# Kernel optimization log

Hardware: AMD Instinct MI355X
Metric: run time of the kernel (lower is better)

The kernel has to match this reference:

```python
import jax, jax.numpy as jnp
import numpy as np

CELL = 128
STEPS = 20
N_KEYS = 4   # ['first_conn','second_conn','first_op','second_op']
N_OUT = 6


def setup_inputs() -> dict:
    key = jax.random.key(0)
    ks = jax.random.split(key, 10)
    s = 0.05
    return {
        "net": jax.random.randint(ks[0], (STEPS,), 0, N_OUT),          # sampled actions, each in [0,6)
        "reward": jax.random.uniform(ks[1], (1,), dtype=jnp.float32),   # unused in forward (kept for signature parity)
        "emb_start": jax.random.normal(ks[2], (1, CELL), jnp.float32) * s,          # Embedding(1,128)
        "emb_keys": jax.random.normal(ks[3], (N_KEYS, N_OUT, CELL), jnp.float32) * s,
        "fc_W": jax.random.normal(ks[4], (N_KEYS, N_OUT, CELL), jnp.float32) * s,
        "fc_b": jax.random.normal(ks[5], (N_KEYS, N_OUT), jnp.float32) * s,
        "W_ih": jax.random.normal(ks[6], (4 * CELL, CELL), jnp.float32) * s,  # LSTMCell input weights (i,f,g,o)
        "W_hh": jax.random.normal(ks[7], (4 * CELL, CELL), jnp.float32) * s,  # LSTMCell hidden weights
        "b_ih": jax.random.normal(ks[8], (4 * CELL,), jnp.float32) * s,
        "b_hh": jax.random.normal(ks[9], (4 * CELL,), jnp.float32) * s,
    }


def _lstm_cell(x, h, c, W_ih, W_hh, b_ih, b_hh):
    # PyTorch LSTMCell: gates ordered (i, f, g, o)
    gates = x @ W_ih.T + b_ih + h @ W_hh.T + b_hh   # [1, 4*CELL]
    i, f, g, o = jnp.split(gates, 4, axis=-1)
    c_new = jax.nn.sigmoid(f) * c + jax.nn.sigmoid(i) * jnp.tanh(g)
    h_new = jax.nn.sigmoid(o) * jnp.tanh(c_new)
    return h_new, c_new


def reference(net, reward, emb_start, emb_keys, fc_W, fc_b, W_ih, W_hh, b_ih, b_hh):
    key_idx = jnp.arange(STEPS) % N_KEYS            # which head/embedding at each step
    fc_W_t = fc_W[key_idx]                          # [STEPS, 6, CELL]
    fc_b_t = fc_b[key_idx]                          # [STEPS, 6]
    emb_t = emb_keys[key_idx, net]                  # [STEPS, CELL] next-step input embedding

    def step(carry, xs):
        h, c, x = carry
        Wt, bt, ev = xs
        h, c = _lstm_cell(x, h, c, W_ih, W_hh, b_ih, b_hh)
        probs = jax.nn.softmax(h @ Wt.T + bt, axis=1)   # [1, 6]
        return (h, c, ev[None, :]), probs

    h0 = jnp.zeros((1, CELL), dtype=emb_start.dtype)
    c0 = jnp.zeros((1, CELL), dtype=emb_start.dtype)
    x0 = emb_start                                   # embedding lookup of action 0 in a 1-row table
    _, outputs = jax.lax.scan(step, (h0, c0, x0), (fc_W_t, fc_b_t, emb_t))
    return outputs                                   # [STEPS, 1, 6], stacked version of the torch list
```

## Files before the change

### kernel.cpp

```cpp
#include <hip/hip_runtime.h>
#include <hip/hip_fp16.h>

#define CELL 128
#define STEPS 20

typedef _Float16 half8_t __attribute__((ext_vector_type(8)));
typedef float    floatx4 __attribute__((ext_vector_type(4)));

#define WS_GX    0
#define WS_WHH   40960
#define WS_FCW   (40960 + 131072)
#define WS_FCB   (WS_FCW + 6144)
#define WS_NEED  (WS_FCB + 96)

__device__ __forceinline__ unsigned packf2(float x, float y) {
    typedef _Float16 h2 __attribute__((ext_vector_type(2)));
    h2 h = { (_Float16)x, (_Float16)y };
    return __builtin_bit_cast(unsigned, h);
}
__device__ __forceinline__ float fdot2u(unsigned a, unsigned b, float c) {
    typedef _Float16 h2 __attribute__((ext_vector_type(2)));
#if __has_builtin(__builtin_amdgcn_fdot2)
    return __builtin_amdgcn_fdot2(__builtin_bit_cast(h2, a), __builtin_bit_cast(h2, b), c, false);
#else
    h2 x = __builtin_bit_cast(h2, a), y = __builtin_bit_cast(h2, b);
    return fmaf((float)x[0], (float)y[0], fmaf((float)x[1], (float)y[1], c));
#endif
}
__device__ __forceinline__ float fastrcp(float x) {
#if __has_builtin(__builtin_amdgcn_rcpf)
    return __builtin_amdgcn_rcpf(x);
#else
    return 1.0f / x;
#endif
}
__device__ __forceinline__ float sig_rcp(float x)  { return fastrcp(1.0f + __expf(-x)); }
__device__ __forceinline__ float tanh_rcp(float x) { return fmaf(2.0f, fastrcp(1.0f + __expf(-2.0f * x)), -1.0f); }
__device__ __forceinline__ half8_t cvt8(const float* p) {
    const float4* p4 = (const float4*)p;
    float4 a = p4[0], b = p4[1];
    return half8_t{ (_Float16)a.x, (_Float16)a.y, (_Float16)a.z, (_Float16)a.w,
                    (_Float16)b.x, (_Float16)b.y, (_Float16)b.z, (_Float16)b.w };
}

extern "C" __global__ void __launch_bounds__(256)
nas_prep_kernel(const int* __restrict__ net,
                const float* __restrict__ emb_start,
                const float* __restrict__ emb_keys,
                const float* __restrict__ fc_W,
                const float* __restrict__ fc_b,
                const float* __restrict__ W_ih,
                const float* __restrict__ W_hh,
                const float* __restrict__ b_ih,
                const float* __restrict__ b_hh,
                unsigned char* __restrict__ ws)
{
    const int b = blockIdx.x, tid = threadIdx.x;

    if (b < 128) {
        __shared__ float sx[STEPS][CELL];
        for (int i = tid; i < STEPS * CELL; i += 256) {
            const int t = i >> 7, k = i & 127;
            sx[t][k] = (t == 0) ? emb_start[k]
                     : emb_keys[((((t - 1) & 3) * 6) + net[t - 1]) * CELL + k];
        }
        __syncthreads();
        const int row  = b * 4 + (tid >> 6);
        const int lane = tid & 63;
        const float2 w = ((const float2*)W_ih)[row * 64 + lane];
        const float bias = b_ih[row] + b_hh[row];
        const int tau = row >> 7, cell = row & 127;
        float* gx = (float*)(ws + WS_GX);
#pragma unroll
        for (int t = 0; t < STEPS; ++t) {
            const float2 xv = *(const float2*)&sx[t][lane * 2];
            float p = fmaf(w.x, xv.x, w.y * xv.y);
            p += __shfl_down(p, 32); p += __shfl_down(p, 16);
            p += __shfl_down(p, 8);  p += __shfl_down(p, 4);
            p += __shfl_down(p, 2);  p += __shfl_down(p, 1);
            if (lane == 0) gx[t * 512 + cell * 4 + tau] = p + bias;
        }
    } else if (b < 160) {
        const int F   = (b - 128) * 256 + tid;
        const int g   = F >> 9;
        const int m   = F & 511;
        const int tau = g >> 2, kc = g & 3;
        const int rr0 = ((m >> 6) << 4) + (m & 15);
        const int qd  = (m >> 4) & 3;
        const int k0  = kc * 32 + qd * 8;
        half8_t h8 = cvt8(W_hh + (tau * 128 + rr0) * CELL + k0);
        ((uint4*)(ws + WS_WHH))[g * 512 + m] = __builtin_bit_cast(uint4, h8);
    } else {
        const float2* fw2 = (const float2*)fc_W;
        unsigned* fcw = (unsigned*)(ws + WS_FCW);
        for (int i = tid; i < 24 * 64; i += 256) {
            const float2 w = fw2[i];
            fcw[i] = packf2(w.x, w.y);
        }
        if (tid < 24) ((float*)(ws + WS_FCB))[tid] = fc_b[tid];
    }
}

extern "C" __global__ void __launch_bounds__(512, 1)
nas_policy_kernel(const unsigned char* __restrict__ ws,
                  float* __restrict__ out)
{
    const int t0   = threadIdx.x;
    const int wv   = t0 >> 6;
    const int lane = t0 & 63;
    const int quad = lane >> 4;
    const int lcol = lane & 15;
    const int rr0  = (wv << 4) + lcol;

    __shared__ __align__(16) _Float16 hbuf[2 * 128];
    __shared__ float llog[STEPS * 8];

    const float*    ws_gx  = (const float*)(ws + WS_GX);
    const uint4*    ws_whh = (const uint4*)(ws + WS_WHH);
    const unsigned* ws_fcw = (const unsigned*)(ws + WS_FCW);
    const float*    ws_fcb = (const float*)(ws + WS_FCB);

    half8_t bf0[4], bf1[4], bf2[4], bf3[4];
#pragma unroll
    for (int kc = 0; kc < 4; ++kc) {
        bf0[kc] = __builtin_bit_cast(half8_t, ws_whh[(0 * 4 + kc) * 512 + t0]);
        bf1[kc] = __builtin_bit_cast(half8_t, ws_whh[(1 * 4 + kc) * 512 + t0]);
        bf2[kc] = __builtin_bit_cast(half8_t, ws_whh[(2 * 4 + kc) * 512 + t0]);
        bf3[kc] = __builtin_bit_cast(half8_t, ws_whh[(3 * 4 + kc) * 512 + t0]);
    }
    if (t0 < 128) hbuf[128 + t0] = (_Float16)0.0f;
    floatx4 gx_cur = *(const floatx4*)&ws_gx[rr0 * 4];
    float c = 0.0f;
    __syncthreads();

    for (int t = 0; t < STEPS; ++t) {
        const uint4* hp4 = (const uint4*)(hbuf + (((t + 1) & 1) << 7));
        const floatx4 gx = gx_cur;
        if (t + 1 < STEPS)
            gx_cur = *(const floatx4*)&ws_gx[(t + 1) * 512 + rr0 * 4];

        floatx4 a0a = { gx[0], 0, 0, 0 }, a0b = { 0, 0, 0, 0 };
        floatx4 a1a = { gx[1], 0, 0, 0 }, a1b = { 0, 0, 0, 0 };
        floatx4 a2a = { gx[2], 0, 0, 0 }, a2b = { 0, 0, 0, 0 };
        floatx4 a3a = { gx[3], 0, 0, 0 }, a3b = { 0, 0, 0, 0 };
        {
            uint4 u0 = hp4[(0 << 2) + quad], u1 = hp4[(1 << 2) + quad];
            uint4 u2 = hp4[(2 << 2) + quad], u3 = hp4[(3 << 2) + quad];
            half8_t f0 = __builtin_bit_cast(half8_t, u0), f1 = __builtin_bit_cast(half8_t, u1);
            half8_t f2 = __builtin_bit_cast(half8_t, u2), f3 = __builtin_bit_cast(half8_t, u3);
            a0a = __builtin_amdgcn_mfma_f32_16x16x32_f16(f0, bf0[0], a0a, 0, 0, 0);
            a1a = __builtin_amdgcn_mfma_f32_16x16x32_f16(f0, bf1[0], a1a, 0, 0, 0);
            a2a = __builtin_amdgcn_mfma_f32_16x16x32_f16(f0, bf2[0], a2a, 0, 0, 0);
            a3a = __builtin_amdgcn_mfma_f32_16x16x32_f16(f0, bf3[0], a3a, 0, 0, 0);
            a0b = __builtin_amdgcn_mfma_f32_16x16x32_f16(f1, bf0[1], a0b, 0, 0, 0);
            a1b = __builtin_amdgcn_mfma_f32_16x16x32_f16(f1, bf1[1], a1b, 0, 0, 0);
            a2b = __builtin_amdgcn_mfma_f32_16x16x32_f16(f1, bf2[1], a2b, 0, 0, 0);
            a3b = __builtin_amdgcn_mfma_f32_16x16x32_f16(f1, bf3[1], a3b, 0, 0, 0);
            a0a = __builtin_amdgcn_mfma_f32_16x16x32_f16(f2, bf0[2], a0a, 0, 0, 0);
            a1a = __builtin_amdgcn_mfma_f32_16x16x32_f16(f2, bf1[2], a1a, 0, 0, 0);
            a2a = __builtin_amdgcn_mfma_f32_16x16x32_f16(f2, bf2[2], a2a, 0, 0, 0);
            a3a = __builtin_amdgcn_mfma_f32_16x16x32_f16(f2, bf3[2], a3a, 0, 0, 0);
            a0b = __builtin_amdgcn_mfma_f32_16x16x32_f16(f3, bf0[3], a0b, 0, 0, 0);
            a1b = __builtin_amdgcn_mfma_f32_16x16x32_f16(f3, bf1[3], a1b, 0, 0, 0);
            a2b = __builtin_amdgcn_mfma_f32_16x16x32_f16(f3, bf2[3], a2b, 0, 0, 0);
            a3b = __builtin_amdgcn_mfma_f32_16x16x32_f16(f3, bf3[3], a3b, 0, 0, 0);
        }

        if (t >= 1 && wv < 6 && quad == 1) {
            const int li = lcol;
            const int hg = ((t - 1) & 3) * 6 + wv;
            const unsigned* hb = (const unsigned*)(hbuf + (((t + 1) & 1) << 7));
            const uint4 wpv = *(const uint4*)(ws_fcw + hg * 64 + li * 4);
            float p = fdot2u(hb[li * 4],     wpv.x, 0.0f);
            p = fdot2u(hb[li * 4 + 1], wpv.y, p);
            p = fdot2u(hb[li * 4 + 2], wpv.z, p);
            p = fdot2u(hb[li * 4 + 3], wpv.w, p);
            p += __shfl_down(p, 8); p += __shfl_down(p, 4);
            p += __shfl_down(p, 2); p += __shfl_down(p, 1);
            if (li == 0) llog[(t - 1) * 8 + wv] = p + ws_fcb[hg];
        }

        {
            float ig = sig_rcp (a0a[0] + a0b[0]);
            float fg = sig_rcp (a1a[0] + a1b[0]);
            float gg = tanh_rcp(a2a[0] + a2b[0]);
            float og = sig_rcp (a3a[0] + a3b[0]);
            c = fg * c + ig * gg;
            float h = og * tanh_rcp(c);
            if (quad == 0)
                hbuf[((t & 1) << 7) + rr0] = (_Float16)h;
        }

        __syncthreads();
    }

    if (wv < 6 && quad == 1) {
        const int li = lcol;
        const int hg = (19 & 3) * 6 + wv;
        const unsigned* hb = (const unsigned*)(hbuf + 128);
        const uint4 wpv = *(const uint4*)(ws_fcw + hg * 64 + li * 4);
        float p = fdot2u(hb[li * 4],     wpv.x, 0.0f);
        p = fdot2u(hb[li * 4 + 1], wpv.y, p);
        p = fdot2u(hb[li * 4 + 2], wpv.z, p);
        p = fdot2u(hb[li * 4 + 3], wpv.w, p);
        p += __shfl_down(p, 8); p += __shfl_down(p, 4);
        p += __shfl_down(p, 2); p += __shfl_down(p, 1);
        if (li == 0) llog[19 * 8 + wv] = p + ws_fcb[hg];
    }
    __syncthreads();
    if (t0 < STEPS * 6) {
        const int s = t0 / 6, k = t0 - s * 6;
        const float* L = llog + s * 8;
        float l0 = L[0], l1 = L[1], l2 = L[2], l3 = L[3], l4 = L[4], l5 = L[5];
        float m = fmaxf(fmaxf(fmaxf(l0, l1), fmaxf(l2, l3)), fmaxf(l4, l5));
        float e0 = __expf(l0 - m), e1 = __expf(l1 - m), e2 = __expf(l2 - m);
        float e3 = __expf(l3 - m), e4 = __expf(l4 - m), e5 = __expf(l5 - m);
        float sum = ((e0 + e1) + (e2 + e3)) + (e4 + e5);
        float mine = (k == 0) ? e0 : (k == 1) ? e1 : (k == 2) ? e2
                   : (k == 3) ? e3 : (k == 4) ? e4 : e5;
        out[t0] = mine / sum;
    }
}

extern "C" __global__ void __launch_bounds__(512, 1)
nas_policy_mono(const int* __restrict__ net,
                const float* __restrict__ emb_start,
                const float* __restrict__ emb_keys,
                const float* __restrict__ fc_W,
                const float* __restrict__ fc_b,
                const float* __restrict__ W_ih,
                const float* __restrict__ W_hh,
                const float* __restrict__ b_ih,
                const float* __restrict__ b_hh,
                float* __restrict__ out)
{
    const int t0   = threadIdx.x;
    const int wv   = t0 >> 6;
    const int lane = t0 & 63;
    const int quad = lane >> 4;
    const int lcol = lane & 15;

    __shared__ __align__(16) unsigned  s_xv2[32 * 68];
    __shared__ __align__(16) float     s_gx[STEPS * 512];
    __shared__ __align__(16) _Float16  hbuf[2 * 128];
    __shared__ unsigned s_fcw2[24 * 64];
    __shared__ float    s_fcb[24];
    __shared__ float    llog[STEPS * 8];

    for (int i = t0; i < STEPS * 64; i += 512) {
        const int m = i >> 6, j = i & 63;
        const float2* src = (m == 0) ? (const float2*)emb_start
            : (const float2*)(emb_keys + ((((m - 1) & 3) * 6) + net[m - 1]) * CELL);
        float2 v = src[j];
        s_xv2[m * 68 + j] = packf2(v.x, v.y);
    }
    {
        const float2* fw2 = (const float2*)fc_W;
        for (int i = t0; i < 24 * 64; i += 512) { float2 w = fw2[i]; s_fcw2[i] = packf2(w.x, w.y); }
    }
    if (t0 < 24)  s_fcb[t0] = fc_b[t0];
    if (t0 < 128) hbuf[128 + t0] = (_Float16)0.0f;

    const int rr0 = (wv << 4) + lcol;
    float biasx[4];
#pragma unroll
    for (int tau = 0; tau < 4; ++tau) {
        const int r = tau * 128 + rr0;
        biasx[tau] = b_ih[r] + b_hh[r];
    }

    __syncthreads();

    {
        half8_t bw[4][4];
#pragma unroll
        for (int kc = 0; kc < 4; ++kc) {
            const int k0 = kc * 32 + quad * 8;
#pragma unroll
            for (int tau = 0; tau < 4; ++tau)
                bw[kc][tau] = cvt8(W_ih + (tau * 128 + rr0) * CELL + k0);
        }
        floatx4 ax0[4] = { {0,0,0,0}, {0,0,0,0}, {0,0,0,0}, {0,0,0,0} };
        floatx4 ax1[4] = { {0,0,0,0}, {0,0,0,0}, {0,0,0,0}, {0,0,0,0} };
#pragma unroll
        for (int kc = 0; kc < 4; ++kc) {
            uint4 u0 = *(const uint4*)&s_xv2[lcol * 68 + kc * 16 + quad * 4];
            uint4 u1 = *(const uint4*)&s_xv2[(16 + lcol) * 68 + kc * 16 + quad * 4];
            half8_t a0f = __builtin_bit_cast(half8_t, u0);
            half8_t a1f = __builtin_bit_cast(half8_t, u1);
#pragma unroll
            for (int tau = 0; tau < 4; ++tau) {
                ax0[tau] = __builtin_amdgcn_mfma_f32_16x16x32_f16(a0f, bw[kc][tau], ax0[tau], 0, 0, 0);
                ax1[tau] = __builtin_amdgcn_mfma_f32_16x16x32_f16(a1f, bw[kc][tau], ax1[tau], 0, 0, 0);
            }
        }
#pragma unroll
        for (int tau = 0; tau < 4; ++tau) {
#pragma unroll
            for (int reg = 0; reg < 4; ++reg)
                s_gx[(quad * 4 + reg) * 512 + rr0 * 4 + tau] = ax0[tau][reg] + biasx[tau];
            if (quad == 0) {
#pragma unroll
                for (int reg = 0; reg < 4; ++reg)
                    s_gx[(16 + reg) * 512 + rr0 * 4 + tau] = ax1[tau][reg] + biasx[tau];
            }
        }
    }

    half8_t bf0[4], bf1[4], bf2[4], bf3[4];
#pragma unroll
    for (int kc = 0; kc < 4; ++kc) {
        const int k0 = kc * 32 + quad * 8;
        bf0[kc] = cvt8(W_hh + (0 * 128 + rr0) * CELL + k0);
        bf1[kc] = cvt8(W_hh + (1 * 128 + rr0) * CELL + k0);
        bf2[kc] = cvt8(W_hh + (2 * 128 + rr0) * CELL + k0);
        bf3[kc] = cvt8(W_hh + (3 * 128 + rr0) * CELL + k0);
    }

    float c = 0.0f;
    __syncthreads();

    for (int t = 0; t < STEPS; ++t) {
        const uint4* hp4 = (const uint4*)(hbuf + (((t + 1) & 1) << 7));
        floatx4 gx = *(const floatx4*)&s_gx[t * 512 + rr0 * 4];
        floatx4 a0a = {0,0,0,0}, a0b = {0,0,0,0}, a1a = {0,0,0,0}, a1b = {0,0,0,0};
        floatx4 a2a = {0,0,0,0}, a2b = {0,0,0,0}, a3a = {0,0,0,0}, a3b = {0,0,0,0};
        {
            uint4 u0 = hp4[(0 << 2) + quad], u1 = hp4[(1 << 2) + quad];
            uint4 u2 = hp4[(2 << 2) + quad], u3 = hp4[(3 << 2) + quad];
            half8_t f0 = __builtin_bit_cast(half8_t, u0), f1 = __builtin_bit_cast(half8_t, u1);
            half8_t f2 = __builtin_bit_cast(half8_t, u2), f3 = __builtin_bit_cast(half8_t, u3);
            a0a = __builtin_amdgcn_mfma_f32_16x16x32_f16(f0, bf0[0], a0a, 0, 0, 0);
            a1a = __builtin_amdgcn_mfma_f32_16x16x32_f16(f0, bf1[0], a1a, 0, 0, 0);
            a2a = __builtin_amdgcn_mfma_f32_16x16x32_f16(f0, bf2[0], a2a, 0, 0, 0);
            a3a = __builtin_amdgcn_mfma_f32_16x16x32_f16(f0, bf3[0], a3a, 0, 0, 0);
            a0b = __builtin_amdgcn_mfma_f32_16x16x32_f16(f1, bf0[1], a0b, 0, 0, 0);
            a1b = __builtin_amdgcn_mfma_f32_16x16x32_f16(f1, bf1[1], a1b, 0, 0, 0);
            a2b = __builtin_amdgcn_mfma_f32_16x16x32_f16(f1, bf2[1], a2b, 0, 0, 0);
            a3b = __builtin_amdgcn_mfma_f32_16x16x32_f16(f1, bf3[1], a3b, 0, 0, 0);
            a0a = __builtin_amdgcn_mfma_f32_16x16x32_f16(f2, bf0[2], a0a, 0, 0, 0);
            a1a = __builtin_amdgcn_mfma_f32_16x16x32_f16(f2, bf1[2], a1a, 0, 0, 0);
            a2a = __builtin_amdgcn_mfma_f32_16x16x32_f16(f2, bf2[2], a2a, 0, 0, 0);
            a3a = __builtin_amdgcn_mfma_f32_16x16x32_f16(f2, bf3[2], a3a, 0, 0, 0);
            a0b = __builtin_amdgcn_mfma_f32_16x16x32_f16(f3, bf0[3], a0b, 0, 0, 0);
            a1b = __builtin_amdgcn_mfma_f32_16x16x32_f16(f3, bf1[3], a1b, 0, 0, 0);
            a2b = __builtin_amdgcn_mfma_f32_16x16x32_f16(f3, bf2[3], a2b, 0, 0, 0);
            a3b = __builtin_amdgcn_mfma_f32_16x16x32_f16(f3, bf3[3], a3b, 0, 0, 0);
        }

        if (t >= 1 && wv < 6 && quad == 1) {
            const int li = lcol;
            const int hg = ((t - 1) & 3) * 6 + wv;
            const unsigned* hb = (const unsigned*)(hbuf + (((t + 1) & 1) << 7));
            const unsigned* wp = s_fcw2 + hg * 64 + li * 4;
            float p = fdot2u(hb[li * 4],     wp[0], 0.0f);
            p = fdot2u(hb[li * 4 + 1], wp[1], p);
            p = fdot2u(hb[li * 4 + 2], wp[2], p);
            p = fdot2u(hb[li * 4 + 3], wp[3], p);
            p += __shfl_down(p, 8); p += __shfl_down(p, 4);
            p += __shfl_down(p, 2); p += __shfl_down(p, 1);
            if (li == 0) llog[(t - 1) * 8 + wv] = p + s_fcb[hg];
        }

        {
            float ig = sig_rcp (a0a[0] + a0b[0] + gx[0]);
            float fg = sig_rcp (a1a[0] + a1b[0] + gx[1]);
            float gg = tanh_rcp(a2a[0] + a2b[0] + gx[2]);
            float og = sig_rcp (a3a[0] + a3b[0] + gx[3]);
            c = fg * c + ig * gg;
            float h = og * tanh_rcp(c);
            if (quad == 0)
                hbuf[((t & 1) << 7) + rr0] = (_Float16)h;
        }

        __syncthreads();
    }

    if (wv < 6 && quad == 1) {
        const int li = lcol;
        const int hg = (19 & 3) * 6 + wv;
        const unsigned* hb = (const unsigned*)(hbuf + 128);
        const unsigned* wp = s_fcw2 + hg * 64 + li * 4;
        float p = fdot2u(hb[li * 4],     wp[0], 0.0f);
        p = fdot2u(hb[li * 4 + 1], wp[1], p);
        p = fdot2u(hb[li * 4 + 2], wp[2], p);
        p = fdot2u(hb[li * 4 + 3], wp[3], p);
        p += __shfl_down(p, 8); p += __shfl_down(p, 4);
        p += __shfl_down(p, 2); p += __shfl_down(p, 1);
        if (li == 0) llog[19 * 8 + wv] = p + s_fcb[hg];
    }
    __syncthreads();
    if (t0 < STEPS * 6) {
        const int s = t0 / 6, k = t0 - s * 6;
        const float* L = llog + s * 8;
        float l0 = L[0], l1 = L[1], l2 = L[2], l3 = L[3], l4 = L[4], l5 = L[5];
        float m = fmaxf(fmaxf(fmaxf(l0, l1), fmaxf(l2, l3)), fmaxf(l4, l5));
        float e0 = __expf(l0 - m), e1 = __expf(l1 - m), e2 = __expf(l2 - m);
        float e3 = __expf(l3 - m), e4 = __expf(l4 - m), e5 = __expf(l5 - m);
        float sum = ((e0 + e1) + (e2 + e3)) + (e4 + e5);
        float mine = (k == 0) ? e0 : (k == 1) ? e1 : (k == 2) ? e2
                   : (k == 3) ? e3 : (k == 4) ? e4 : e5;
        out[t0] = mine / sum;
    }
}

extern "C" void kernel_launch(void* const* d_in, const int* in_sizes, int n_in,
                              void* d_out, int out_size, void* d_ws, size_t ws_size,
                              hipStream_t stream) {
    (void)in_sizes; (void)n_in; (void)out_size;
    const int*   net       = (const int*)d_in[0];
    const float* emb_start = (const float*)d_in[2];
    const float* emb_keys  = (const float*)d_in[3];
    const float* fc_W      = (const float*)d_in[4];
    const float* fc_b      = (const float*)d_in[5];
    const float* W_ih      = (const float*)d_in[6];
    const float* W_hh      = (const float*)d_in[7];
    const float* b_ih      = (const float*)d_in[8];
    const float* b_hh      = (const float*)d_in[9];
    float*       out       = (float*)d_out;

    if (d_ws != nullptr && ws_size >= (size_t)WS_NEED) {
        unsigned char* ws = (unsigned char*)d_ws;
        hipLaunchKernelGGL(nas_prep_kernel, dim3(161), dim3(256), 0, stream,
                           net, emb_start, emb_keys, fc_W, fc_b,
                           W_ih, W_hh, b_ih, b_hh, ws);
        hipLaunchKernelGGL(nas_policy_kernel, dim3(1), dim3(512), 0, stream,
                           (const unsigned char*)ws, out);
    } else {
        hipLaunchKernelGGL(nas_policy_mono, dim3(1), dim3(512), 0, stream,
                           net, emb_start, emb_keys, fc_W, fc_b,
                           W_ih, W_hh, b_ih, b_hh, out);
    }
}
```

Before: 97.32 us.

## Break MFMA accumulator chains, skip step-0 matmul, lighter LDS barriers

Splits the recurrent-matmul accumulators into 16 independent chains so the MFMAs no longer wait on each other, and fully unrolls the 20-step loop. Step 0 skips the matmul because h is zero, which also removes the hbuf zero-init and its barrier. Input-gate projections are now prefetched two steps ahead. Each __syncthreads is replaced with an inline-asm lgkmcnt wait plus s_barrier, and the prep kernel's barrier is moved after its global weight loads so they overlap. Costs are more registers for the extra accumulators and reliance on the hand-written barrier being enough for correctness.

```diff
diff --git a/kernel.cpp b/kernel.cpp
--- a/kernel.cpp
+++ b/kernel.cpp
@@ -41,6 +41,9 @@
     float4 a = p4[0], b = p4[1];
     return half8_t{ (_Float16)a.x, (_Float16)a.y, (_Float16)a.z, (_Float16)a.w,
                     (_Float16)b.x, (_Float16)b.y, (_Float16)b.z, (_Float16)b.w };
+}
+__device__ __forceinline__ void bar_lds() {
+    asm volatile("s_waitcnt lgkmcnt(0)\n\ts_barrier" ::: "memory");
 }
 
 extern "C" __global__ void __launch_bounds__(256)
@@ -64,11 +67,11 @@
             sx[t][k] = (t == 0) ? emb_start[k]
                      : emb_keys[((((t - 1) & 3) * 6) + net[t - 1]) * CELL + k];
         }
-        __syncthreads();
         const int row  = b * 4 + (tid >> 6);
         const int lane = tid & 63;
         const float2 w = ((const float2*)W_ih)[row * 64 + lane];
         const float bias = b_ih[row] + b_hh[row];
+        __syncthreads();
         const int tau = row >> 7, cell = row & 127;
         float* gx = (float*)(ws + WS_GX);
 #pragma unroll
@@ -128,70 +131,80 @@
         bf2[kc] = __builtin_bit_cast(half8_t, ws_whh[(2 * 4 + kc) * 512 + t0]);
         bf3[kc] = __builtin_bit_cast(half8_t, ws_whh[(3 * 4 + kc) * 512 + t0]);
     }
-    if (t0 < 128) hbuf[128 + t0] = (_Float16)0.0f;
-    floatx4 gx_cur = *(const floatx4*)&ws_gx[rr0 * 4];
+
+    floatx4 gxA = *(const floatx4*)&ws_gx[0 * 512 + rr0 * 4];
+    floatx4 gxB = *(const floatx4*)&ws_gx[1 * 512 + rr0 * 4];
     float c = 0.0f;
-    __syncthreads();
-
+
+#pragma unroll
     for (int t = 0; t < STEPS; ++t) {
-        const uint4* hp4 = (const uint4*)(hbuf + (((t + 1) & 1) << 7));
-        const floatx4 gx = gx_cur;
-        if (t + 1 < STEPS)
-            gx_cur = *(const floatx4*)&ws_gx[(t + 1) * 512 + rr0 * 4];
-
-        floatx4 a0a = { gx[0], 0, 0, 0 }, a0b = { 0, 0, 0, 0 };
-        floatx4 a1a = { gx[1], 0, 0, 0 }, a1b = { 0, 0, 0, 0 };
-        floatx4 a2a = { gx[2], 0, 0, 0 }, a2b = { 0, 0, 0, 0 };
-        floatx4 a3a = { gx[3], 0, 0, 0 }, a3b = { 0, 0, 0, 0 };
-        {
+        const floatx4 gx = gxA;
+        gxA = gxB;
+        if (t + 2 < STEPS)
+            gxB = *(const floatx4*)&ws_gx[(t + 2) * 512 + rr0 * 4];
+
+        float s0, s1, s2, s3;
+        if (t == 0) {
+            s0 = gx[0]; s1 = gx[1]; s2 = gx[2]; s3 = gx[3];
+        } else {
+            const uint4* hp4 = (const uint4*)(hbuf + (((t + 1) & 1) << 7));
             uint4 u0 = hp4[(0 << 2) + quad], u1 = hp4[(1 << 2) + quad];
             uint4 u2 = hp4[(2 << 2) + quad], u3 = hp4[(3 << 2) + quad];
             half8_t f0 = __builtin_bit_cast(half8_t, u0), f1 = __builtin_bit_cast(half8_t, u1);
             half8_t f2 = __builtin_bit_cast(half8_t, u2), f3 = __builtin_bit_cast(half8_t, u3);
-            a0a = __builtin_amdgcn_mfma_f32_16x16x32_f16(f0, bf0[0], a0a, 0, 0, 0);
-            a1a = __builtin_amdgcn_mfma_f32_16x16x32_f16(f0, bf1[0], a1a, 0, 0, 0);
-            a2a = __builtin_amdgcn_mfma_f32_16x16x32_f16(f0, bf2[0], a2a, 0, 0, 0);
-            a3a = __builtin_amdgcn_mfma_f32_16x16x32_f16(f0, bf3[0], a3a, 0, 0, 0);
-            a0b = __builtin_amdgcn_mfma_f32_16x16x32_f16(f1, bf0[1], a0b, 0, 0, 0);
-            a1b = __builtin_amdgcn_mfma_f32_16x16x32_f16(f1, bf1[1], a1b, 0, 0, 0);
-            a2b = __builtin_amdgcn_mfma_f32_16x16x32_f16(f1, bf2[1], a2b, 0, 0, 0);
-            a3b = __builtin_amdgcn_mfma_f32_16x16x32_f16(f1, bf3[1], a3b, 0, 0, 0);
-            a0a = __builtin_amdgcn_mfma_f32_16x16x32_f16(f2, bf0[2], a0a, 0, 0, 0);
-            a1a = __builtin_amdgcn_mfma_f32_16x16x32_f16(f2, bf1[2], a1a, 0, 0, 0);
-            a2a = __builtin_amdgcn_mfma_f32_16x16x32_f16(f2, bf2[2], a2a, 0, 0, 0);
-            a3a = __builtin_amdgcn_mfma_f32_16x16x32_f16(f2, bf3[2], a3a, 0, 0, 0);
-            a0b = __builtin_amdgcn_mfma_f32_16x16x32_f16(f3, bf0[3], a0b, 0, 0, 0);
-            a1b = __builtin_amdgcn_mfma_f32_16x16x32_f16(f3, bf1[3], a1b, 0, 0, 0);
-            a2b = __builtin_amdgcn_mfma_f32_16x16x32_f16(f3, bf2[3], a2b, 0, 0, 0);
-            a3b = __builtin_amdgcn_mfma_f32_16x16x32_f16(f3, bf3[3], a3b, 0, 0, 0);
-        }
-
-        if (t >= 1 && wv < 6 && quad == 1) {
-            const int li = lcol;
-            const int hg = ((t - 1) & 3) * 6 + wv;
-            const unsigned* hb = (const unsigned*)(hbuf + (((t + 1) & 1) << 7));
-            const uint4 wpv = *(const uint4*)(ws_fcw + hg * 64 + li * 4);
-            float p = fdot2u(hb[li * 4],     wpv.x, 0.0f);
-            p = fdot2u(hb[li * 4 + 1], wpv.y, p);
-            p = fdot2u(hb[li * 4 + 2], wpv.z, p);
-            p = fdot2u(hb[li * 4 + 3], wpv.w, p);
-            p += __shfl_down(p, 8); p += __shfl_down(p, 4);
-            p += __shfl_down(p, 2); p += __shfl_down(p, 1);
-            if (li == 0) llog[(t - 1) * 8 + wv] = p + ws_fcb[hg];
+            floatx4 a00 = {0,0,0,0}, a01 = {0,0,0,0}, a02 = {0,0,0,0}, a03 = {0,0,0,0};
+            floatx4 a10 = {0,0,0,0}, a11 = {0,0,0,0}, a12 = {0,0,0,0}, a13 = {0,0,0,0};
+            floatx4 a20 = {0,0,0,0}, a21 = {0,0,0,0}, a22 = {0,0,0,0}, a23 = {0,0,0,0};
+            floatx4 a30 = {0,0,0,0}, a31 = {0,0,0,0}, a32 = {0,0,0,0}, a33 = {0,0,0,0};
+            a00 = __builtin_amdgcn_mfma_f32_16x16x32_f16(f0, bf0[0], a00, 0, 0, 0);
+            a10 = __builtin_amdgcn_mfma_f32_16x16x32_f16(f0, bf1[0], a10, 0, 0, 0);
+            a20 = __builtin_amdgcn_mfma_f32_16x16x32_f16(f0, bf2[0], a20, 0, 0, 0);
+            a30 = __builtin_amdgcn_mfma_f32_16x16x32_f16(f0, bf3[0], a30, 0, 0, 0);
+            a01 = __builtin_amdgcn_mfma_f32_16x16x32_f16(f1, bf0[1], a01, 0, 0, 0);
+            a11 = __builtin_amdgcn_mfma_f32_16x16x32_f16(f1, bf1[1], a11, 0, 0, 0);
+            a21 = __builtin_amdgcn_mfma_f32_16x16x32_f16(f1, bf2[1], a21, 0, 0, 0);
+            a31 = __builtin_amdgcn_mfma_f32_16x16x32_f16(f1, bf3[1], a31, 0, 0, 0);
+            a02 = __builtin_amdgcn_mfma_f32_16x16x32_f16(f2, bf0[2], a02, 0, 0, 0);
+            a12 = __builtin_amdgcn_mfma_f32_16x16x32_f16(f2, bf1[2], a12, 0, 0, 0);
+            a22 = __builtin_amdgcn_mfma_f32_16x16x32_f16(f2, bf2[2], a22, 0, 0, 0);
+            a32 = __builtin_amdgcn_mfma_f32_16x16x32_f16(f2, bf3[2], a32, 0, 0, 0);
+            a03 = __builtin_amdgcn_mfma_f32_16x16x32_f16(f3, bf0[3], a03, 0, 0, 0);
+            a13 = __builtin_amdgcn_mfma_f32_16x16x32_f16(f3, bf1[3], a13, 0, 0, 0);
+            a23 = __builtin_amdgcn_mfma_f32_16x16x32_f16(f3, bf2[3], a23, 0, 0, 0);
+            a33 = __builtin_amdgcn_mfma_f32_16x16x32_f16(f3, bf3[3], a33, 0, 0, 0);
+
+            if (wv < 6 && quad == 1) {
+                const int li = lcol;
+                const int hg = ((t - 1) & 3) * 6 + wv;
+                const unsigned* hb = (const unsigned*)(hbuf + (((t + 1) & 1) << 7));
+                const uint4 wpv = *(const uint4*)(ws_fcw + hg * 64 + li * 4);
+                float p = fdot2u(hb[li * 4],     wpv.x, 0.0f);
+                p = fdot2u(hb[li * 4 + 1], wpv.y, p);
+                p = fdot2u(hb[li * 4 + 2], wpv.z, p);
+                p = fdot2u(hb[li * 4 + 3], wpv.w, p);
+                p += __shfl_down(p, 8); p += __shfl_down(p, 4);
+                p += __shfl_down(p, 2); p += __shfl_down(p, 1);
+                if (li == 0) llog[(t - 1) * 8 + wv] = p + ws_fcb[hg];
+            }
+
+            s0 = (a00[0] + a01[0]) + (a02[0] + a03[0]) + gx[0];
+            s1 = (a10[0] + a11[0]) + (a12[0] + a13[0]) + gx[1];
+            s2 = (a20[0] + a21[0]) + (a22[0] + a23[0]) + gx[2];
+            s3 = (a30[0] + a31[0]) + (a32[0] + a33[0]) + gx[3];
         }
 
         {
-            float ig = sig_rcp (a0a[0] + a0b[0]);
-            float fg = sig_rcp (a1a[0] + a1b[0]);
-            float gg = tanh_rcp(a2a[0] + a2b[0]);
-            float og = sig_rcp (a3a[0] + a3b[0]);
+            float ig = sig_rcp (s0);
+            float fg = sig_rcp (s1);
+            float gg = tanh_rcp(s2);
+            float og = sig_rcp (s3);
             c = fg * c + ig * gg;
             float h = og * tanh_rcp(c);
             if (quad == 0)
                 hbuf[((t & 1) << 7) + rr0] = (_Float16)h;
         }
 
-        __syncthreads();
+        bar_lds();
     }
 
     if (wv < 6 && quad == 1) {
@@ -207,7 +220,7 @@
         p += __shfl_down(p, 2); p += __shfl_down(p, 1);
         if (li == 0) llog[19 * 8 + wv] = p + ws_fcb[hg];
     }
-    __syncthreads();
+    bar_lds();
     if (t0 < STEPS * 6) {
         const int s = t0 / 6, k = t0 - s * 6;
         const float* L = llog + s * 8;
```

New measurement: 99.41 us. 1.02x slower.

## Fuse prep and policy kernels into one cooperative launch with grid sync

Applied to the files above, without the earlier changes.

Merges the two-kernel pipeline (parallel prep of input gates and fp16 W_hh layout, then a single-block recurrent LSTM) into one cooperative kernel of 81 blocks. A grid.sync separates the phases, after which block 0 runs the recurrence. The FC head weights are staged in block 0's shared memory during the prep phase. This removes one kernel launch and its inter-kernel gap, at the cost of grid-sync overhead and a cooperative-launch requirement, with a fallback to the old path if that launch fails.

```diff
diff --git a/kernel.cpp b/kernel.cpp
--- a/kernel.cpp
+++ b/kernel.cpp
@@ -1,5 +1,8 @@
 #include <hip/hip_runtime.h>
 #include <hip/hip_fp16.h>
+#include <hip/hip_cooperative_groups.h>
+
+namespace cg = cooperative_groups;
 
 #define CELL 128
 #define STEPS 20
@@ -41,6 +44,185 @@
     float4 a = p4[0], b = p4[1];
     return half8_t{ (_Float16)a.x, (_Float16)a.y, (_Float16)a.z, (_Float16)a.w,
                     (_Float16)b.x, (_Float16)b.y, (_Float16)b.z, (_Float16)b.w };
+}
+
+extern "C" __global__ void __launch_bounds__(512, 1)
+nas_fused_kernel(const int* __restrict__ net,
+                 const float* __restrict__ emb_start,
+                 const float* __restrict__ emb_keys,
+                 const float* __restrict__ fc_W,
+                 const float* __restrict__ fc_b,
+                 const float* __restrict__ W_ih,
+                 const float* __restrict__ W_hh,
+                 const float* __restrict__ b_ih,
+                 const float* __restrict__ b_hh,
+                 unsigned char* __restrict__ ws,
+                 float* __restrict__ out)
+{
+    cg::grid_group grid = cg::this_grid();
+    const int b   = blockIdx.x;
+    const int tid = threadIdx.x;
+
+    __shared__ __align__(16) float     sx[STEPS][CELL];
+    __shared__ __align__(16) _Float16  hbuf[2 * 128];
+    __shared__ __align__(16) unsigned  s_fcw2[24 * 64];
+    __shared__ float s_fcb[24];
+    __shared__ float llog[STEPS * 8];
+
+    if (b >= 1 && b <= 64) {
+        for (int i = tid; i < STEPS * CELL; i += 512) {
+            const int t = i >> 7, k = i & 127;
+            sx[t][k] = (t == 0) ? emb_start[k]
+                     : emb_keys[((((t - 1) & 3) * 6) + net[t - 1]) * CELL + k];
+        }
+        const int row  = (b - 1) * 8 + (tid >> 6);
+        const int lane = tid & 63;
+        const float2 w = ((const float2*)W_ih)[row * 64 + lane];
+        const float bias = b_ih[row] + b_hh[row];
+        __syncthreads();
+        const int tau = row >> 7, cell = row & 127;
+        float* gx = (float*)(ws + WS_GX);
+#pragma unroll
+        for (int t = 0; t < STEPS; ++t) {
+            const float2 xv = *(const float2*)&sx[t][lane * 2];
+            float p = fmaf(w.x, xv.x, w.y * xv.y);
+            p += __shfl_down(p, 32); p += __shfl_down(p, 16);
+            p += __shfl_down(p, 8);  p += __shfl_down(p, 4);
+            p += __shfl_down(p, 2);  p += __shfl_down(p, 1);
+            if (lane == 0) gx[t * 512 + cell * 4 + tau] = p + bias;
+        }
+    } else if (b >= 65) {
+        const int F   = (b - 65) * 512 + tid;
+        const int g   = F >> 9;
+        const int m   = F & 511;
+        const int tau = g >> 2, kc = g & 3;
+        const int rr0 = ((m >> 6) << 4) + (m & 15);
+        const int qd  = (m >> 4) & 3;
+        const int k0  = kc * 32 + qd * 8;
+        half8_t h8 = cvt8(W_hh + (tau * 128 + rr0) * CELL + k0);
+        ((uint4*)(ws + WS_WHH))[g * 512 + m] = __builtin_bit_cast(uint4, h8);
+    } else {
+        const float2* fw2 = (const float2*)fc_W;
+        for (int i = tid; i < 24 * 64; i += 512) {
+            const float2 w = fw2[i];
+            s_fcw2[i] = packf2(w.x, w.y);
+        }
+        if (tid < 24) s_fcb[tid] = fc_b[tid];
+    }
+
+    grid.sync();
+    if (b != 0) return;
+
+    const int t0   = tid;
+    const int wv   = t0 >> 6;
+    const int lane = t0 & 63;
+    const int quad = lane >> 4;
+    const int lcol = lane & 15;
+    const int rr0  = (wv << 4) + lcol;
+
+    const float* ws_gx  = (const float*)(ws + WS_GX);
+    const uint4* ws_whh = (const uint4*)(ws + WS_WHH);
+
+    half8_t bf0[4], bf1[4], bf2[4], bf3[4];
+#pragma unroll
+    for (int kc = 0; kc < 4; ++kc) {
+        bf0[kc] = __builtin_bit_cast(half8_t, ws_whh[(0 * 4 + kc) * 512 + t0]);
+        bf1[kc] = __builtin_bit_cast(half8_t, ws_whh[(1 * 4 + kc) * 512 + t0]);
+        bf2[kc] = __builtin_bit_cast(half8_t, ws_whh[(2 * 4 + kc) * 512 + t0]);
+        bf3[kc] = __builtin_bit_cast(half8_t, ws_whh[(3 * 4 + kc) * 512 + t0]);
+    }
+    if (t0 < 128) hbuf[128 + t0] = (_Float16)0.0f;
+    floatx4 gx_cur = *(const floatx4*)&ws_gx[rr0 * 4];
+    float c = 0.0f;
+    __syncthreads();
+
+    for (int t = 0; t < STEPS; ++t) {
+        const uint4* hp4 = (const uint4*)(hbuf + (((t + 1) & 1) << 7));
+        const floatx4 gx = gx_cur;
+        if (t + 1 < STEPS)
+            gx_cur = *(const floatx4*)&ws_gx[(t + 1) * 512 + rr0 * 4];
+
+        floatx4 a0a = { gx[0], 0, 0, 0 }, a0b = { 0, 0, 0, 0 };
+        floatx4 a1a = { gx[1], 0, 0, 0 }, a1b = { 0, 0, 0, 0 };
+        floatx4 a2a = { gx[2], 0, 0, 0 }, a2b = { 0, 0, 0, 0 };
+        floatx4 a3a = { gx[3], 0, 0, 0 }, a3b = { 0, 0, 0, 0 };
+        {
+            uint4 u0 = hp4[(0 << 2) + quad], u1 = hp4[(1 << 2) + quad];
+            uint4 u2 = hp4[(2 << 2) + quad], u3 = hp4[(3 << 2) + quad];
+            half8_t f0 = __builtin_bit_cast(half8_t, u0), f1 = __builtin_bit_cast(half8_t, u1);
+            half8_t f2 = __builtin_bit_cast(half8_t, u2), f3 = __builtin_bit_cast(half8_t, u3);
+            a0a = __builtin_amdgcn_mfma_f32_16x16x32_f16(f0, bf0[0], a0a, 0, 0, 0);
+            a1a = __builtin_amdgcn_mfma_f32_16x16x32_f16(f0, bf1[0], a1a, 0, 0, 0);
+            a2a = __builtin_amdgcn_mfma_f32_16x16x32_f16(f0, bf2[0], a2a, 0, 0, 0);
+            a3a = __builtin_amdgcn_mfma_f32_16x16x32_f16(f0, bf3[0], a3a, 0, 0, 0);
+            a0b = __builtin_amdgcn_mfma_f32_16x16x32_f16(f1, bf0[1], a0b, 0, 0, 0);
+            a1b = __builtin_amdgcn_mfma_f32_16x16x32_f16(f1, bf1[1], a1b, 0, 0, 0);
+            a2b = __builtin_amdgcn_mfma_f32_16x16x32_f16(f1, bf2[1], a2b, 0, 0, 0);
+            a3b = __builtin_amdgcn_mfma_f32_16x16x32_f16(f1, bf3[1], a3b, 0, 0, 0);
+            a0a = __builtin_amdgcn_mfma_f32_16x16x32_f16(f2, bf0[2], a0a, 0, 0, 0);
+            a1a = __builtin_amdgcn_mfma_f32_16x16x32_f16(f2, bf1[2], a1a, 0, 0, 0);
+            a2a = __builtin_amdgcn_mfma_f32_16x16x32_f16(f2, bf2[2], a2a, 0, 0, 0);
+            a3a = __builtin_amdgcn_mfma_f32_16x16x32_f16(f2, bf3[2], a3a, 0, 0, 0);
+            a0b = __builtin_amdgcn_mfma_f32_16x16x32_f16(f3, bf0[3], a0b, 0, 0, 0);
+            a1b = __builtin_amdgcn_mfma_f32_16x16x32_f16(f3, bf1[3], a1b, 0, 0, 0);
+            a2b = __builtin_amdgcn_mfma_f32_16x16x32_f16(f3, bf2[3], a2b, 0, 0, 0);
+            a3b = __builtin_amdgcn_mfma_f32_16x16x32_f16(f3, bf3[3], a3b, 0, 0, 0);
+        }
+
+        if (t >= 1 && wv < 6 && quad == 1) {
+            const int li = lcol;
+            const int hg = ((t - 1) & 3) * 6 + wv;
+            const unsigned* hb = (const unsigned*)(hbuf + (((t + 1) & 1) << 7));
+            const uint4 wpv = *(const uint4*)(s_fcw2 + hg * 64 + li * 4);
+            float p = fdot2u(hb[li * 4],     wpv.x, 0.0f);
+            p = fdot2u(hb[li * 4 + 1], wpv.y, p);
+            p = fdot2u(hb[li * 4 + 2], wpv.z, p);
+            p = fdot2u(hb[li * 4 + 3], wpv.w, p);
+            p += __shfl_down(p, 8); p += __shfl_down(p, 4);
+            p += __shfl_down(p, 2); p += __shfl_down(p, 1);
+            if (li == 0) llog[(t - 1) * 8 + wv] = p + s_fcb[hg];
+        }
+
+        {
+            float ig = sig_rcp (a0a[0] + a0b[0]);
+            float fg = sig_rcp (a1a[0] + a1b[0]);
+            float gg = tanh_rcp(a2a[0] + a2b[0]);
+            float og = sig_rcp (a3a[0] + a3b[0]);
+            c = fg * c + ig * gg;
+            float h = og * tanh_rcp(c);
+            if (quad == 0)
+                hbuf[((t & 1) << 7) + rr0] = (_Float16)h;
+        }
+
+        __syncthreads();
+    }
+
+    if (wv < 6 && quad == 1) {
+        const int li = lcol;
+        const int hg = (19 & 3) * 6 + wv;
+        const unsigned* hb = (const unsigned*)(hbuf + 128);
+        const uint4 wpv = *(const uint4*)(s_fcw2 + hg * 64 + li * 4);
+        float p = fdot2u(hb[li * 4],     wpv.x, 0.0f);
+        p = fdot2u(hb[li * 4 + 1], wpv.y, p);
+        p = fdot2u(hb[li * 4 + 2], wpv.z, p);
+        p = fdot2u(hb[li * 4 + 3], wpv.w, p);
+        p += __shfl_down(p, 8); p += __shfl_down(p, 4);
+        p += __shfl_down(p, 2); p += __shfl_down(p, 1);
+        if (li == 0) llog[19 * 8 + wv] = p + s_fcb[hg];
+    }
+    __syncthreads();
+    if (t0 < STEPS * 6) {
+        const int s = t0 / 6, k = t0 - s * 6;
+        const float* L = llog + s * 8;
+        float l0 = L[0], l1 = L[1], l2 = L[2], l3 = L[3], l4 = L[4], l5 = L[5];
+        float m = fmaxf(fmaxf(fmaxf(l0, l1), fmaxf(l2, l3)), fmaxf(l4, l5));
+        float e0 = __expf(l0 - m), e1 = __expf(l1 - m), e2 = __expf(l2 - m);
+        float e3 = __expf(l3 - m), e4 = __expf(l4 - m), e5 = __expf(l5 - m);
+        float sum = ((e0 + e1) + (e2 + e3)) + (e4 + e5);
+        float mine = (k == 0) ? e0 : (k == 1) ? e1 : (k == 2) ? e2
+                   : (k == 3) ? e3 : (k == 4) ? e4 : e5;
+        out[t0] = mine / sum;
+    }
 }
 
 extern "C" __global__ void __launch_bounds__(256)
@@ -64,11 +246,11 @@
             sx[t][k] = (t == 0) ? emb_start[k]
                      : emb_keys[((((t - 1) & 3) * 6) + net[t - 1]) * CELL + k];
         }
-        __syncthreads();
         const int row  = b * 4 + (tid >> 6);
         const int lane = tid & 63;
         const float2 w = ((const float2*)W_ih)[row * 64 + lane];
         const float bias = b_ih[row] + b_hh[row];
+        __syncthreads();
         const int tau = row >> 7, cell = row & 127;
         float* gx = (float*)(ws + WS_GX);
 #pragma unroll
@@ -421,11 +603,20 @@
 
     if (d_ws != nullptr && ws_size >= (size_t)WS_NEED) {
         unsigned char* ws = (unsigned char*)d_ws;
-        hipLaunchKernelGGL(nas_prep_kernel, dim3(161), dim3(256), 0, stream,
-                           net, emb_start, emb_keys, fc_W, fc_b,
-                           W_ih, W_hh, b_ih, b_hh, ws);
-        hipLaunchKernelGGL(nas_policy_kernel, dim3(1), dim3(512), 0, stream,
-                           (const unsigned char*)ws, out);
+        void* kargs[] = {
+            (void*)&net, (void*)&emb_start, (void*)&emb_keys, (void*)&fc_W,
+            (void*)&fc_b, (void*)&W_ih, (void*)&W_hh, (void*)&b_ih,
+            (void*)&b_hh, (void*)&ws, (void*)&out
+        };
+        hipError_t err = hipLaunchCooperativeKernel(
+            (const void*)nas_fused_kernel, dim3(81), dim3(512), kargs, 0, stream);
+        if (err != hipSuccess) {
+            hipLaunchKernelGGL(nas_prep_kernel, dim3(161), dim3(256), 0, stream,
+                               net, emb_start, emb_keys, fc_W, fc_b,
+                               W_ih, W_hh, b_ih, b_hh, ws);
+            hipLaunchKernelGGL(nas_policy_kernel, dim3(1), dim3(512), 0, stream,
+                               (const unsigned char*)ws, out);
+        }
     } else {
         hipLaunchKernelGGL(nas_policy_mono, dim3(1), dim3(512), 0, stream,
                            net, emb_start, emb_keys, fc_W, fc_b,
```

After: 132.2 us. +35.9%, slower.

## Fuse prep and recurrent kernels into one launch with flag-based inter-block signaling

Applied to the files above, without the earlier changes.

Replaces the two-kernel prep+policy sequence with a single 81-block launch. Helper blocks compute the input-gate projections and fp16 W_hh fragments and publish them with release-store magic flags. Block 0 spin-waits on those flags, with timeout fallbacks that recompute locally, and starts the recurrence once the first 10 timesteps of gx are ready. FC weights are packed into shared memory instead of the workspace. This removes one kernel launch and lets prep overlap the recurrence, but it relies on co-residency of the blocks, spin-wait polling and flag reset at kernel end.

```diff
diff --git a/kernel.cpp b/kernel.cpp
--- a/kernel.cpp
+++ b/kernel.cpp
@@ -3,15 +3,15 @@
 
 #define CELL 128
 #define STEPS 20
+#define MAGIC 0x5F3A9C21u
 
 typedef _Float16 half8_t __attribute__((ext_vector_type(8)));
 typedef float    floatx4 __attribute__((ext_vector_type(4)));
 
 #define WS_GX    0
 #define WS_WHH   40960
-#define WS_FCW   (40960 + 131072)
-#define WS_FCB   (WS_FCW + 6144)
-#define WS_NEED  (WS_FCB + 96)
+#define WS_FLG   172032
+#define WS_NEED  (172032 + 144 * 4)
 
 __device__ __forceinline__ unsigned packf2(float x, float y) {
     typedef _Float16 h2 __attribute__((ext_vector_type(2)));
@@ -43,97 +43,191 @@
                     (_Float16)b.x, (_Float16)b.y, (_Float16)b.z, (_Float16)b.w };
 }
 
-extern "C" __global__ void __launch_bounds__(256)
-nas_prep_kernel(const int* __restrict__ net,
-                const float* __restrict__ emb_start,
-                const float* __restrict__ emb_keys,
-                const float* __restrict__ fc_W,
-                const float* __restrict__ fc_b,
-                const float* __restrict__ W_ih,
-                const float* __restrict__ W_hh,
-                const float* __restrict__ b_ih,
-                const float* __restrict__ b_hh,
-                unsigned char* __restrict__ ws)
+__device__ static void self_gx(float (*sx)[CELL], const int* net,
+                               const float* emb_start, const float* emb_keys,
+                               const float* W_ih, const float* b_ih, const float* b_hh,
+                               float* gxp, int tid, int tlo)
 {
-    const int b = blockIdx.x, tid = threadIdx.x;
-
-    if (b < 128) {
-        __shared__ float sx[STEPS][CELL];
-        for (int i = tid; i < STEPS * CELL; i += 256) {
+    for (int i = tid; i < STEPS * CELL; i += 512) {
+        const int t = i >> 7, k = i & 127;
+        sx[t][k] = (t == 0) ? emb_start[k]
+                 : emb_keys[((((t - 1) & 3) * 6) + net[t - 1]) * CELL + k];
+    }
+    __syncthreads();
+    const int row = tid, tau = row >> 7, cell = row & 127;
+    const float4* w4 = (const float4*)(W_ih + row * CELL);
+    const float bias = b_ih[row] + b_hh[row];
+    for (int t = tlo; t < STEPS; ++t) {
+        const float4* x4 = (const float4*)sx[t];
+        float a = 0.f, b = 0.f, c = 0.f, d = 0.f;
+#pragma unroll 8
+        for (int k = 0; k < 32; ++k) {
+            float4 wv = w4[k], xv = x4[k];
+            a = fmaf(wv.x, xv.x, a); b = fmaf(wv.y, xv.y, b);
+            c = fmaf(wv.z, xv.z, c); d = fmaf(wv.w, xv.w, d);
+        }
+        gxp[t * 512 + cell * 4 + tau] = (a + b) + (c + d) + bias;
+    }
+    __threadfence();
+    __syncthreads();
+}
+
+extern "C" __global__ void __launch_bounds__(512, 1)
+nas_fused_kernel(const int* __restrict__ net,
+                 const float* __restrict__ emb_start,
+                 const float* __restrict__ emb_keys,
+                 const float* __restrict__ fc_W,
+                 const float* __restrict__ fc_b,
+                 const float* __restrict__ W_ih,
+                 const float* __restrict__ W_hh,
+                 const float* __restrict__ b_ih,
+                 const float* __restrict__ b_hh,
+                 unsigned char* __restrict__ ws,
+                 float* __restrict__ out)
+{
+    const int b   = blockIdx.x;
+    const int tid = threadIdx.x;
+
+    __shared__ __align__(16) float     sx[STEPS][CELL];
+    __shared__ __align__(16) _Float16  hbuf[2 * 128];
+    __shared__ __align__(16) unsigned  s_fcw2[24 * 64];
+    __shared__ float s_fcb[24];
+    __shared__ float llog[STEPS * 8];
+    __shared__ int   s_fail[3];
+
+    unsigned* flg = (unsigned*)(ws + WS_FLG);
+    float*    gxp = (float*)(ws + WS_GX);
+
+    if (b >= 1 && b <= 64) {
+        for (int i = tid; i < STEPS * CELL; i += 512) {
             const int t = i >> 7, k = i & 127;
             sx[t][k] = (t == 0) ? emb_start[k]
                      : emb_keys[((((t - 1) & 3) * 6) + net[t - 1]) * CELL + k];
         }
-        __syncthreads();
-        const int row  = b * 4 + (tid >> 6);
+        const int row  = (b - 1) * 8 + (tid >> 6);
         const int lane = tid & 63;
         const float2 w = ((const float2*)W_ih)[row * 64 + lane];
         const float bias = b_ih[row] + b_hh[row];
+        __syncthreads();
         const int tau = row >> 7, cell = row & 127;
-        float* gx = (float*)(ws + WS_GX);
-#pragma unroll
-        for (int t = 0; t < STEPS; ++t) {
+#pragma unroll
+        for (int t = 0; t < 10; ++t) {
             const float2 xv = *(const float2*)&sx[t][lane * 2];
             float p = fmaf(w.x, xv.x, w.y * xv.y);
             p += __shfl_down(p, 32); p += __shfl_down(p, 16);
             p += __shfl_down(p, 8);  p += __shfl_down(p, 4);
             p += __shfl_down(p, 2);  p += __shfl_down(p, 1);
-            if (lane == 0) gx[t * 512 + cell * 4 + tau] = p + bias;
-        }
-    } else if (b < 160) {
-        const int F   = (b - 128) * 256 + tid;
+            if (lane == 0) gxp[t * 512 + cell * 4 + tau] = p + bias;
+        }
+        __syncthreads();
+        if (tid == 0)
+            __hip_atomic_store(&flg[16 + (b - 1)], MAGIC, __ATOMIC_RELEASE, __HIP_MEMORY_SCOPE_AGENT);
+#pragma unroll
+        for (int t = 10; t < STEPS; ++t) {
+            const float2 xv = *(const float2*)&sx[t][lane * 2];
+            float p = fmaf(w.x, xv.x, w.y * xv.y);
+            p += __shfl_down(p, 32); p += __shfl_down(p, 16);
+            p += __shfl_down(p, 8);  p += __shfl_down(p, 4);
+            p += __shfl_down(p, 2);  p += __shfl_down(p, 1);
+            if (lane == 0) gxp[t * 512 + cell * 4 + tau] = p + bias;
+        }
+        __syncthreads();
+        if (tid == 0)
+            __hip_atomic_store(&flg[80 + (b - 1)], MAGIC, __ATOMIC_RELEASE, __HIP_MEMORY_SCOPE_AGENT);
+        return;
+    } else if (b >= 65) {
+        const int F   = (b - 65) * 512 + tid;
         const int g   = F >> 9;
         const int m   = F & 511;
         const int tau = g >> 2, kc = g & 3;
-        const int rr0 = ((m >> 6) << 4) + (m & 15);
+        const int rr  = ((m >> 6) << 4) + (m & 15);
         const int qd  = (m >> 4) & 3;
         const int k0  = kc * 32 + qd * 8;
-        half8_t h8 = cvt8(W_hh + (tau * 128 + rr0) * CELL + k0);
+        half8_t h8 = cvt8(W_hh + (tau * 128 + rr) * CELL + k0);
         ((uint4*)(ws + WS_WHH))[g * 512 + m] = __builtin_bit_cast(uint4, h8);
-    } else {
-        const float2* fw2 = (const float2*)fc_W;
-        unsigned* fcw = (unsigned*)(ws + WS_FCW);
-        for (int i = tid; i < 24 * 64; i += 256) {
-            const float2 w = fw2[i];
-            fcw[i] = packf2(w.x, w.y);
-        }
-        if (tid < 24) ((float*)(ws + WS_FCB))[tid] = fc_b[tid];
-    }
-}
-
-extern "C" __global__ void __launch_bounds__(512, 1)
-nas_policy_kernel(const unsigned char* __restrict__ ws,
-                  float* __restrict__ out)
-{
-    const int t0   = threadIdx.x;
+        __syncthreads();
+        if (tid == 0)
+            __hip_atomic_store(&flg[b - 65], MAGIC, __ATOMIC_RELEASE, __HIP_MEMORY_SCOPE_AGENT);
+        return;
+    }
+
+    const int t0   = tid;
     const int wv   = t0 >> 6;
     const int lane = t0 & 63;
     const int quad = lane >> 4;
     const int lcol = lane & 15;
     const int rr0  = (wv << 4) + lcol;
 
-    __shared__ __align__(16) _Float16 hbuf[2 * 128];
-    __shared__ float llog[STEPS * 8];
-
-    const float*    ws_gx  = (const float*)(ws + WS_GX);
-    const uint4*    ws_whh = (const uint4*)(ws + WS_WHH);
-    const unsigned* ws_fcw = (const unsigned*)(ws + WS_FCW);
-    const float*    ws_fcb = (const float*)(ws + WS_FCB);
+    if (tid < 3) s_fail[tid] = 0;
+    {
+        const float2* fw2 = (const float2*)fc_W;
+        for (int i = tid; i < 24 * 64; i += 512) {
+            const float2 w = fw2[i];
+            s_fcw2[i] = packf2(w.x, w.y);
+        }
+        if (tid < 24)  s_fcb[tid] = fc_b[tid];
+        if (tid < 128) hbuf[128 + tid] = (_Float16)0.0f;
+    }
+
+    if (tid < 16) {
+        int budget = 1 << 17;
+        while (__hip_atomic_load(&flg[tid], __ATOMIC_RELAXED, __HIP_MEMORY_SCOPE_AGENT) != MAGIC)
+            if (--budget == 0) { atomicOr(&s_fail[0], 1); break; }
+    }
+    __syncthreads();
+    __builtin_amdgcn_fence(__ATOMIC_ACQUIRE, "agent");
 
     half8_t bf0[4], bf1[4], bf2[4], bf3[4];
-#pragma unroll
-    for (int kc = 0; kc < 4; ++kc) {
-        bf0[kc] = __builtin_bit_cast(half8_t, ws_whh[(0 * 4 + kc) * 512 + t0]);
-        bf1[kc] = __builtin_bit_cast(half8_t, ws_whh[(1 * 4 + kc) * 512 + t0]);
-        bf2[kc] = __builtin_bit_cast(half8_t, ws_whh[(2 * 4 + kc) * 512 + t0]);
-        bf3[kc] = __builtin_bit_cast(half8_t, ws_whh[(3 * 4 + kc) * 512 + t0]);
-    }
-    if (t0 < 128) hbuf[128 + t0] = (_Float16)0.0f;
+    if (s_fail[0] == 0) {
+        const uint4* ws_whh = (const uint4*)(ws + WS_WHH);
+#pragma unroll
+        for (int kc = 0; kc < 4; ++kc) {
+            bf0[kc] = __builtin_bit_cast(half8_t, ws_whh[(0 * 4 + kc) * 512 + t0]);
+            bf1[kc] = __builtin_bit_cast(half8_t, ws_whh[(1 * 4 + kc) * 512 + t0]);
+            bf2[kc] = __builtin_bit_cast(half8_t, ws_whh[(2 * 4 + kc) * 512 + t0]);
+            bf3[kc] = __builtin_bit_cast(half8_t, ws_whh[(3 * 4 + kc) * 512 + t0]);
+        }
+    } else {
+#pragma unroll
+        for (int kc = 0; kc < 4; ++kc) {
+            const int k0 = kc * 32 + quad * 8;
+            bf0[kc] = cvt8(W_hh + (0 * 128 + rr0) * CELL + k0);
+            bf1[kc] = cvt8(W_hh + (1 * 128 + rr0) * CELL + k0);
+            bf2[kc] = cvt8(W_hh + (2 * 128 + rr0) * CELL + k0);
+            bf3[kc] = cvt8(W_hh + (3 * 128 + rr0) * CELL + k0);
+        }
+    }
+
+    if (tid < 64) {
+        int budget = 1 << 17;
+        while (__hip_atomic_load(&flg[16 + tid], __ATOMIC_RELAXED, __HIP_MEMORY_SCOPE_AGENT) != MAGIC)
+            if (--budget == 0) { atomicOr(&s_fail[1], 1); break; }
+    }
+    __syncthreads();
+    __builtin_amdgcn_fence(__ATOMIC_ACQUIRE, "agent");
+    bool need_b = true;
+    if (s_fail[1]) {
+        self_gx(sx, net, emb_start, emb_keys, W_ih, b_ih, b_hh, gxp, tid, 0);
+        need_b = false;
+    }
+
+    const float* ws_gx = (const float*)(ws + WS_GX);
     floatx4 gx_cur = *(const floatx4*)&ws_gx[rr0 * 4];
     float c = 0.0f;
-    __syncthreads();
 
     for (int t = 0; t < STEPS; ++t) {
+        if (t == 9 && need_b) {
+            if (tid < 64) {
+                int budget = 1 << 20;
+                while (__hip_atomic_load(&flg[80 + tid], __ATOMIC_RELAXED, __HIP_MEMORY_SCOPE_AGENT) != MAGIC)
+                    if (--budget == 0) { atomicOr(&s_fail[2], 1); break; }
+            }
+            __syncthreads();
+            __builtin_amdgcn_fence(__ATOMIC_ACQUIRE, "agent");
+            if (s_fail[2])
+                self_gx(sx, net, emb_start, emb_keys, W_ih, b_ih, b_hh, gxp, tid, 10);
+        }
+
         const uint4* hp4 = (const uint4*)(hbuf + (((t + 1) & 1) << 7));
         const floatx4 gx = gx_cur;
         if (t + 1 < STEPS)
@@ -170,14 +264,14 @@
             const int li = lcol;
             const int hg = ((t - 1) & 3) * 6 + wv;
             const unsigned* hb = (const unsigned*)(hbuf + (((t + 1) & 1) << 7));
-            const uint4 wpv = *(const uint4*)(ws_fcw + hg * 64 + li * 4);
+            const uint4 wpv = *(const uint4*)(s_fcw2 + hg * 64 + li * 4);
             float p = fdot2u(hb[li * 4],     wpv.x, 0.0f);
             p = fdot2u(hb[li * 4 + 1], wpv.y, p);
             p = fdot2u(hb[li * 4 + 2], wpv.z, p);
             p = fdot2u(hb[li * 4 + 3], wpv.w, p);
             p += __shfl_down(p, 8); p += __shfl_down(p, 4);
             p += __shfl_down(p, 2); p += __shfl_down(p, 1);
-            if (li == 0) llog[(t - 1) * 8 + wv] = p + ws_fcb[hg];
+            if (li == 0) llog[(t - 1) * 8 + wv] = p + s_fcb[hg];
         }
 
         {
@@ -198,14 +292,14 @@
         const int li = lcol;
         const int hg = (19 & 3) * 6 + wv;
         const unsigned* hb = (const unsigned*)(hbuf + 128);
-        const uint4 wpv = *(const uint4*)(ws_fcw + hg * 64 + li * 4);
+        const uint4 wpv = *(const uint4*)(s_fcw2 + hg * 64 + li * 4);
         float p = fdot2u(hb[li * 4],     wpv.x, 0.0f);
         p = fdot2u(hb[li * 4 + 1], wpv.y, p);
         p = fdot2u(hb[li * 4 + 2], wpv.z, p);
         p = fdot2u(hb[li * 4 + 3], wpv.w, p);
         p += __shfl_down(p, 8); p += __shfl_down(p, 4);
         p += __shfl_down(p, 2); p += __shfl_down(p, 1);
-        if (li == 0) llog[19 * 8 + wv] = p + ws_fcb[hg];
+        if (li == 0) llog[19 * 8 + wv] = p + s_fcb[hg];
     }
     __syncthreads();
     if (t0 < STEPS * 6) {
@@ -220,6 +314,10 @@
                    : (k == 3) ? e3 : (k == 4) ? e4 : e5;
         out[t0] = mine / sum;
     }
+
+    if (t0 < 144) flg[t0] = 0u;
+    __syncthreads();
+    if (t0 == 0) __builtin_amdgcn_fence(__ATOMIC_RELEASE, "agent");
 }
 
 extern "C" __global__ void __launch_bounds__(512, 1)
@@ -421,11 +519,9 @@
 
     if (d_ws != nullptr && ws_size >= (size_t)WS_NEED) {
         unsigned char* ws = (unsigned char*)d_ws;
-        hipLaunchKernelGGL(nas_prep_kernel, dim3(161), dim3(256), 0, stream,
+        hipLaunchKernelGGL(nas_fused_kernel, dim3(81), dim3(512), 0, stream,
                            net, emb_start, emb_keys, fc_W, fc_b,
-                           W_ih, W_hh, b_ih, b_hh, ws);
-        hipLaunchKernelGGL(nas_policy_kernel, dim3(1), dim3(512), 0, stream,
-                           (const unsigned char*)ws, out);
+                           W_ih, W_hh, b_ih, b_hh, ws, out);
     } else {
         hipLaunchKernelGGL(nas_policy_mono, dim3(1), dim3(512), 0, stream,
                            net, emb_start, emb_keys, fc_W, fc_b,
```

Measured after the change: 93.48 us. -3.9%, faster.
